# Kernel tuning notes

Hardware: AMD Instinct MI355X
Metric: run time of the kernel (lower is better)

The kernel has to match this reference:

```python
import jax, jax.numpy as jnp
import numpy as np


def setup_inputs() -> dict:
    key = jax.random.key(0)
    B, T, D = 16, 2048, 256
    inputs = jax.random.normal(key, (B, T, D), dtype=jnp.float32)
    return {"inputs": inputs, "window_size": 7}


def reference(inputs, window_size):
    # Faithful to the keras layer: output[b, t] = concat(x[t], x[t-1], ..., x[t-W+1])
    # with zeros where t-k < 0. Built with one pad + W shifted views instead of
    # the original O(W^2) pad/concat loop.
    B, T, D = inputs.shape
    W = window_size
    padded = jnp.pad(inputs, ((0, 0), (W - 1, 0), (0, 0)))  # [B, T+W-1, D]
    # slice k gives x shifted right by k (i.e., x[t-k]) over the valid range
    pieces = [padded[:, W - 1 - k : W - 1 - k + T, :] for k in range(W)]
    return jnp.concatenate(pieces, axis=2)  # [B, T, W*D]
```

## Files before the change

### kernel.cpp

```cpp
#include <hip/hip_runtime.h>


typedef float vf4 __attribute__((ext_vector_type(4)));

constexpr int B    = 16;
constexpr int T    = 2048;
constexpr int D    = 256;
constexpr int W    = 7;
constexpr int D4   = D / 4;
constexpr int ROW4 = W * D4;
constexpr int G    = 8;
constexpr int NLD  = G + W - 1;
constexpr int NROW = B * T;
constexpr int NWAVE = NROW / G;
constexpr int NBLK  = NWAVE / 4;

__global__ __launch_bounds__(256) void window_waverow_kernel(
    const vf4* __restrict__ in, vf4* __restrict__ out) {
  const int wid  = (blockIdx.x << 2) | (threadIdx.x >> 6);
  const int lane = threadIdx.x & 63;
  const int r0   = wid * G;
  const int t0   = r0 & (T - 1);

  vf4 v[NLD];
  if (t0 != 0) {
    const vf4* src = in + (r0 - (W - 1)) * D4 + lane;
#pragma unroll
    for (int j = 0; j < NLD; ++j) v[j] = src[j * D4];
  } else {
    const vf4 z = {0.f, 0.f, 0.f, 0.f};
#pragma unroll
    for (int j = 0; j < W - 1; ++j) v[j] = z;
    const vf4* src = in + r0 * D4 + lane;
#pragma unroll
    for (int j = 0; j < G; ++j) v[W - 1 + j] = src[j * D4];
  }

  vf4* dst = out + (size_t)r0 * ROW4 + lane;
#pragma unroll
  for (int i = 0; i < G; ++i) {
#pragma unroll
    for (int w = 0; w < W; ++w) {
      dst[i * ROW4 + w * D4] = v[i + (W - 1) - w];
    }
  }
}

extern "C" void kernel_launch(void* const* d_in, const int* in_sizes, int n_in,
                              void* d_out, int out_size, void* d_ws, size_t ws_size,
                              hipStream_t stream) {
  const vf4* in = (const vf4*)d_in[0];
  vf4* out = (vf4*)d_out;
  window_waverow_kernel<<<NBLK, 256, 0, stream>>>(in, out);
}
```

Before: 263.7 us.

## Restructure window kernel so each block stores a contiguous output span linearly

Each block now covers 16 output rows and its 256 threads write the span in consecutive order, with every store reading its source vector straight from global memory through a divmod-by-7 index. Before, each wave loaded 14 input rows into registers and wrote 8 rows with strided per-wave stores. The aim is fully linear, block-wide coalesced stores for this write-bound copy. In exchange, input rows are re-read once per window position (served mostly from cache) and the per-store index arithmetic adds a few instructions.

```diff
diff --git a/kernel.cpp b/kernel.cpp
--- a/kernel.cpp
+++ b/kernel.cpp
@@ -9,39 +9,44 @@
 constexpr int W    = 7;
 constexpr int D4   = D / 4;
 constexpr int ROW4 = W * D4;
-constexpr int G    = 8;
-constexpr int NLD  = G + W - 1;
-constexpr int NROW = B * T;
-constexpr int NWAVE = NROW / G;
-constexpr int NBLK  = NWAVE / 4;
+constexpr int RPB  = 16;
+constexpr int SPAN = RPB * ROW4;
+constexpr int THREADS = 256;
+constexpr int ITER = SPAN / THREADS;
+constexpr int NBLK = B * T / RPB;
 
-__global__ __launch_bounds__(256) void window_waverow_kernel(
+__global__ __launch_bounds__(THREADS) void window_linstore_kernel(
     const vf4* __restrict__ in, vf4* __restrict__ out) {
-  const int wid  = (blockIdx.x << 2) | (threadIdx.x >> 6);
-  const int lane = threadIdx.x & 63;
-  const int r0   = wid * G;
+  const int tid  = threadIdx.x;
+  const int lane = tid & 63;
+  const int wv   = tid >> 6;
+  const int r0   = blockIdx.x * RPB;
   const int t0   = r0 & (T - 1);
 
-  vf4 v[NLD];
+  const vf4* src = in + (size_t)r0 * D4 + lane;
+  vf4* dst = out + (size_t)r0 * ROW4 + tid;
+
   if (t0 != 0) {
-    const vf4* src = in + (r0 - (W - 1)) * D4 + lane;
 #pragma unroll
-    for (int j = 0; j < NLD; ++j) v[j] = src[j * D4];
+    for (int i = 0; i < ITER; ++i) {
+      unsigned s   = (unsigned)(i * 4 + wv);
+      unsigned row = s / 7u;
+      unsigned w   = s - row * 7u;
+      int sr = (int)row - (int)w;
+      vf4 v = src[sr * D4];
+      dst[i * THREADS] = v;
+    }
   } else {
-    const vf4 z = {0.f, 0.f, 0.f, 0.f};
 #pragma unroll
-    for (int j = 0; j < W - 1; ++j) v[j] = z;
-    const vf4* src = in + r0 * D4 + lane;
-#pragma unroll
-    for (int j = 0; j < G; ++j) v[W - 1 + j] = src[j * D4];
-  }
-
-  vf4* dst = out + (size_t)r0 * ROW4 + lane;
-#pragma unroll
-  for (int i = 0; i < G; ++i) {
-#pragma unroll
-    for (int w = 0; w < W; ++w) {
-      dst[i * ROW4 + w * D4] = v[i + (W - 1) - w];
+    for (int i = 0; i < ITER; ++i) {
+      unsigned s   = (unsigned)(i * 4 + wv);
+      unsigned row = s / 7u;
+      unsigned w   = s - row * 7u;
+      int sr = (int)row - (int)w;
+      int srs = sr < 0 ? 0 : sr;
+      vf4 v = src[srs * D4];
+      vf4 z = {0.f, 0.f, 0.f, 0.f};
+      dst[i * THREADS] = (sr >= 0) ? v : z;
     }
   }
 }
@@ -51,5 +56,5 @@
                               hipStream_t stream) {
   const vf4* in = (const vf4*)d_in[0];
   vf4* out = (vf4*)d_out;
-  window_waverow_kernel<<<NBLK, 256, 0, stream>>>(in, out);
+  window_linstore_kernel<<<NBLK, THREADS, 0, stream>>>(in, out);
 }
```

Result: no change. 263.2 us (-0.2%).
